# Kernel tuning notes

Measured on AMD Instinct MI355X. Metric: run time of the kernel, lower is better.

Reference implementation:

```python
import jax, jax.numpy as jnp
import numpy as np

D_MODEL = 1024
NUM_HEADS = 16
D_K = D_MODEL // NUM_HEADS


def setup_inputs() -> dict:
    key = jax.random.key(0)
    ks = jax.random.split(key, 9)
    s = 1.0 / np.sqrt(D_MODEL)
    x = jax.random.normal(ks[0], (2, 2048, D_MODEL), dtype=jnp.float32)
    Wq = jax.random.uniform(ks[1], (D_MODEL, D_MODEL), jnp.float32, -s, s)
    bq = jax.random.uniform(ks[2], (D_MODEL,), jnp.float32, -s, s)
    Wk = jax.random.uniform(ks[3], (D_MODEL, D_MODEL), jnp.float32, -s, s)
    bk = jax.random.uniform(ks[4], (D_MODEL,), jnp.float32, -s, s)
    Wv = jax.random.uniform(ks[5], (D_MODEL, D_MODEL), jnp.float32, -s, s)
    bv = jax.random.uniform(ks[6], (D_MODEL,), jnp.float32, -s, s)
    Wo = jax.random.uniform(ks[7], (D_MODEL, D_MODEL), jnp.float32, -s, s)
    bo = jax.random.uniform(ks[8], (D_MODEL,), jnp.float32, -s, s)
    return {"x": x, "Wq": Wq, "bq": bq, "Wk": Wk, "bk": bk,
            "Wv": Wv, "bv": bv, "Wo": Wo, "bo": bo}


def reference(x, Wq, bq, Wk, bk, Wv, bv, Wo, bo):
    B, S, _ = x.shape
    # torch Linear: y = x @ W.T + b
    def split_heads(t):
        return t.reshape(B, S, NUM_HEADS, D_K).transpose(0, 2, 1, 3)  # [B,H,S,Dk]
    Q = split_heads(x @ Wq.T + bq)
    K = split_heads(x @ Wk.T + bk)
    V = split_heads(x @ Wv.T + bv)
    scale = 1.0 / np.sqrt(D_K).astype(np.float32)
    scores = jnp.einsum('bhqd,bhkd->bhqk', Q, K) * scale  # [B,H,S,S]
    attn = jax.nn.softmax(scores, axis=-1)
    out = jnp.einsum('bhqk,bhkd->bhqd', attn, V)  # [B,H,S,Dk]
    out = out.transpose(0, 2, 1, 3).reshape(B, S, D_MODEL)
    return out @ Wo.T + bo
```

## Files before the change

### kernel.cpp

```cpp
#include <hip/hip_runtime.h>

constexpr int DMODEL = 1024;
constexpr int NHEAD  = 16;
constexpr int DKH    = 64;
constexpr int BATCH  = 2;
constexpr int SEQ    = 2048;
constexpr int MTOT   = BATCH * SEQ;
constexpr float SCL  = 0.18033688011112042f;

typedef __attribute__((ext_vector_type(8)))  short short8;
typedef __attribute__((ext_vector_type(4)))  float floatx4;
typedef __attribute__((ext_vector_type(16))) float floatx16;
typedef __attribute__((ext_vector_type(4)))  uint  uintx4;

__device__ __forceinline__ ushort f2bf(float f) {
    unsigned u = __builtin_bit_cast(unsigned, f);
    u = (u + 0x7fffu + ((u >> 16) & 1u)) >> 16;
    return (ushort)u;
}

__device__ __forceinline__ float exp2n(float x) {
#if __has_builtin(__builtin_amdgcn_exp2f)
    return __builtin_amdgcn_exp2f(x);
#else
    float r;
    asm("v_exp_f32 %0, %1" : "=v"(r) : "v"(x));
    return r;
#endif
}

__device__ __forceinline__ void gld16(const ushort* g, ushort* l) {
    __builtin_amdgcn_global_load_lds(
        (const __attribute__((address_space(1))) void*)g,
        (__attribute__((address_space(3))) void*)l, 16, 0, 0);
}

__global__ __launch_bounds__(256) void cvt_kernel(
    const float* __restrict__ x,  const float* __restrict__ wq,
    const float* __restrict__ wk, const float* __restrict__ wv,
    const float* __restrict__ wo,
    ushort* __restrict__ xb, ushort* __restrict__ wc, ushort* __restrict__ wob) {
    const int id = blockIdx.x * 256 + threadIdx.x;
    const float* src;
    ushort* dst;
    if (id < (1 << 20)) {
        src = x + (size_t)id * 4;
        dst = xb + (size_t)id * 4;
    } else {
        const int t = id - (1 << 20);
        const int seg = t >> 18;
        const size_t off = (size_t)(t & 0x3ffff) * 4;
        src = (seg == 0 ? wq : seg == 1 ? wk : seg == 2 ? wv : wo) + off;
        dst = (seg < 3) ? (wc + ((size_t)seg << 20) + off) : (wob + off);
    }
    const float4 v = *(const float4*)src;
    uint2 o;
    o.x = (uint)f2bf(v.x) | ((uint)f2bf(v.y) << 16);
    o.y = (uint)f2bf(v.z) | ((uint)f2bf(v.w) << 16);
    *(uint2*)dst = o;
}

template <int BMT, int MODE>
__global__ __launch_bounds__(256) void gemm_bf16(
    const ushort* __restrict__ A, const ushort* __restrict__ W,
    const float* __restrict__ bias0, const float* __restrict__ bias1,
    const float* __restrict__ bias2,
    ushort* __restrict__ Oq, ushort* __restrict__ Ok, ushort* __restrict__ Ov,
    float* __restrict__ Of) {
    constexpr int BM = 64 * BMT, BN = 128, BK = 64;
    constexpr int MI = 2 * BMT;
    constexpr int CA = BM / 8, CT = CA + BN / 8, NISS = CT / 4;
    constexpr int NKS = DMODEL / BK;
    __shared__ ushort Als[2][BM * BK];
    __shared__ ushort Bls[2][BN * BK];

    const int tid = threadIdx.x;
    const int w = tid >> 6, l = tid & 63;
    const int lr = l & 15, lg = l >> 4;
    const int wm = w >> 1, wn = w & 1;
    const int m0 = blockIdx.x * BM, n0 = blockIdx.y * BN;

    floatx4 acc[MI][4] = {};

    auto stage = [&](int ks, int buf) {
#pragma unroll
        for (int i = 0; i < NISS; i++) {
            const int c = w * NISS + i;
            const int cc = (c < CA) ? c : c - CA;
            const int row = (cc << 3) + (l >> 3);
            const int gcol = (((l & 7) ^ (row & 7)) << 3);
            if (c < CA)
                gld16(A + (size_t)(m0 + row) * DMODEL + ks * BK + gcol, &Als[buf][cc << 9]);
            else
                gld16(W + (size_t)(n0 + row) * DMODEL + ks * BK + gcol, &Bls[buf][cc << 9]);
        }
    };

    auto compute = [&](int buf) {
#pragma unroll
        for (int kk = 0; kk < 2; kk++) {
            short8 af[MI], bfv[4];
            const int u = kk * 4 + lg;
#pragma unroll
            for (int i = 0; i < MI; i++) {
                const int r = wm * (BM / 2) + i * 16 + lr;
                af[i] = *(const short8*)&Als[buf][r * 64 + ((u ^ (r & 7)) << 3)];
            }
#pragma unroll
            for (int j = 0; j < 4; j++) {
                const int r = wn * 64 + j * 16 + lr;
                bfv[j] = *(const short8*)&Bls[buf][r * 64 + ((u ^ (r & 7)) << 3)];
            }
            __builtin_amdgcn_s_setprio(1);
#pragma unroll
            for (int i = 0; i < MI; i++)
#pragma unroll
                for (int j = 0; j < 4; j++)
                    acc[i][j] = __builtin_amdgcn_mfma_f32_16x16x32_bf16(af[i], bfv[j], acc[i][j], 0, 0, 0);
            __builtin_amdgcn_s_setprio(0);
        }
    };

    stage(0, 0);
    __syncthreads();
#pragma unroll 1
    for (int ks = 0; ks < NKS - 1; ks++) {
        stage(ks + 1, (ks + 1) & 1);
        compute(ks & 1);
        __syncthreads();
    }
    compute((NKS - 1) & 1);

#pragma unroll
    for (int i = 0; i < MI; i++) {
        const int rbase = m0 + wm * (BM / 2) + i * 16 + lg * 4;
#pragma unroll
        for (int j = 0; j < 4; j++) {
            const int cg = n0 + wn * 64 + j * 16 + lr;
            if constexpr (MODE == 1) {
                const float bb = bias0[cg];
#pragma unroll
                for (int p = 0; p < 4; p++)
                    Of[(size_t)(rbase + p) * DMODEL + cg] = acc[i][j][p] + bb;
            } else {
                const int sel = cg >> 10, cw = cg & 1023;
                const int h = cw >> 6, d = cw & 63;
                const float bb = (sel == 0 ? bias0 : sel == 1 ? bias1 : bias2)[cw];
                const int b = rbase >> 11, s = rbase & (SEQ - 1);
                if (sel == 2) {
                    uint2 pk;
                    pk.x = (uint)f2bf(acc[i][j][0] + bb) | ((uint)f2bf(acc[i][j][1] + bb) << 16);
                    pk.y = (uint)f2bf(acc[i][j][2] + bb) | ((uint)f2bf(acc[i][j][3] + bb) << 16);
                    *(uint2*)&Ov[((size_t)(b * NHEAD + h) * DKH + d) * SEQ + s] = pk;
                } else if (sel == 0) {
                    uint2 pk;
                    pk.x = (uint)f2bf((acc[i][j][0] + bb) * SCL) |
                           ((uint)f2bf((acc[i][j][1] + bb) * SCL) << 16);
                    pk.y = (uint)f2bf((acc[i][j][2] + bb) * SCL) |
                           ((uint)f2bf((acc[i][j][3] + bb) * SCL) << 16);
                    *(uint2*)&Oq[((size_t)(b * NHEAD + h) * DKH + d) * SEQ + s] = pk;
                } else {
#pragma unroll
                    for (int p = 0; p < 4; p++)
                        Ok[((size_t)(b * NHEAD + h) * SEQ + s + p) * DKH + d] = f2bf(acc[i][j][p] + bb);
                }
            }
        }
    }
}

__global__ __launch_bounds__(512, 4) void attn_kernel(
    const ushort* __restrict__ Qt, const ushort* __restrict__ K,
    const ushort* __restrict__ Vt, ushort* __restrict__ O) {
    constexpr int KT = 64, NT = SEQ / KT, NTG = NT / 2;
    __shared__ ushort Kls[2][2][KT * 64];
    __shared__ ushort Vls[2][2][KT * 64];

    const int tid = threadIdx.x;
    const int w = tid >> 6, l = tid & 63;
    const int wl = w & 3, wg = w >> 2;
    const int q32 = l & 31, hl = l >> 5, l7 = l & 7;
    const int l0 = blockIdx.x;
    const int bh = (l0 & 7) + ((l0 >> 7) << 3);
    const int q0 = ((l0 >> 3) & 15) * 128;
    const int qb = q0 + wl * 32;
    const ushort* Qh = Qt + (size_t)bh * DKH * SEQ;
    const ushort* Kh = K  + (size_t)bh * SEQ * DKH;
    const ushort* Vh = Vt + (size_t)bh * DKH * SEQ;

    short8 qf[4];
#pragma unroll
    for (int c = 0; c < 4; c++)
#pragma unroll
        for (int j = 0; j < 8; j++)
            ((ushort*)&qf[c])[j] = Qh[(size_t)(16 * c + 8 * hl + j) * SEQ + qb + q32];

    short8 ones;
#pragma unroll
    for (int j = 0; j < 8; j++) ones[j] = (short)0x3F80;

    const int sr8 = l >> 3;
    const int scol = ((l & 7) ^ (sr8 & 7)) * 8;
    const ushort* Kg = Kh + (size_t)(wl * 16 + sr8) * DKH + scol;
    const ushort* Vg = Vh + (size_t)(wl * 16 + sr8) * SEQ + scol;

    floatx16 acc0 = {}, acc1 = {}, accl = {};

    auto stage = [&](int t, int buf) {
        ushort* kd = &Kls[wg][buf][0];
        ushort* vd = &Vls[wg][buf][0];
        gld16(Kg + (size_t)t * (KT * DKH),           kd + wl * 1024);
        gld16(Kg + (size_t)t * (KT * DKH) + 8 * DKH, kd + wl * 1024 + 512);
        gld16(Vg + (size_t)t * KT,                   vd + wl * 1024);
        gld16(Vg + (size_t)t * KT + 8 * SEQ,         vd + wl * 1024 + 512);
    };

    auto compute = [&](int buf) {
        const ushort* kb = &Kls[wg][buf][0];
        const ushort* vb = &Vls[wg][buf][0];
#pragma unroll
        for (int h = 0; h < 2; h++) {
            floatx16 sa = {};
            __builtin_amdgcn_s_setprio(1);
#pragma unroll
            for (int c = 0; c < 4; c++) {
                const int sl = (((2 * c + hl) ^ l7) << 3);
                const short8 kf = *(const short8*)&kb[(h * 32 + q32) * 64 + sl];
                sa = __builtin_amdgcn_mfma_f32_32x32x16_bf16(kf, qf[c], sa, 0, 0, 0);
            }
            __builtin_amdgcn_s_setprio(0);

#pragma unroll
            for (int i = 0; i < 16; i++) sa[i] = exp2n(sa[i]);

            uint wd[8];
#pragma unroll
            for (int m = 0; m < 8; m++)
                asm("v_cvt_pk_bf16_f32 %0, %1, %2"
                    : "=v"(wd[m]) : "v"(sa[2 * m]), "v"(sa[2 * m + 1]));
            asm volatile("v_permlane32_swap_b32 %0, %1" : "+v"(wd[0]), "+v"(wd[2]));
            asm volatile("v_permlane32_swap_b32 %0, %1" : "+v"(wd[1]), "+v"(wd[3]));
            asm volatile("v_permlane32_swap_b32 %0, %1" : "+v"(wd[4]), "+v"(wd[6]));
            asm volatile("v_permlane32_swap_b32 %0, %1" : "+v"(wd[5]), "+v"(wd[7]));
            uintx4 f0 = {wd[0], wd[1], wd[2], wd[3]};
            uintx4 f1 = {wd[4], wd[5], wd[6], wd[7]};
            const short8 pf0 = __builtin_bit_cast(short8, f0);
            const short8 pf1 = __builtin_bit_cast(short8, f1);

            __builtin_amdgcn_s_setprio(1);
#pragma unroll
            for (int c2 = 0; c2 < 2; c2++) {
                const int c = h * 2 + c2;
                const int sl = (((2 * c + hl) ^ l7) << 3);
                const short8 pfc = c2 ? pf1 : pf0;
                const short8 vf0 = *(const short8*)&vb[q32 * 64 + sl];
                const short8 vf1 = *(const short8*)&vb[(32 + q32) * 64 + sl];
                acc0 = __builtin_amdgcn_mfma_f32_32x32x16_bf16(vf0, pfc, acc0, 0, 0, 0);
                acc1 = __builtin_amdgcn_mfma_f32_32x32x16_bf16(vf1, pfc, acc1, 0, 0, 0);
                accl = __builtin_amdgcn_mfma_f32_32x32x16_bf16(ones, pfc, accl, 0, 0, 0);
            }
            __builtin_amdgcn_s_setprio(0);
        }
    };

    const int tb = wg * NTG;
    stage(tb, 0);
    __syncthreads();
#pragma unroll 1
    for (int it = 0; it < NTG / 2 - 1; it++) {
        stage(tb + 2 * it + 1, 1);
        compute(0);
        __syncthreads();
        stage(tb + 2 * it + 2, 0);
        compute(1);
        __syncthreads();
    }
    stage(tb + NTG - 1, 1);
    compute(0);
    __syncthreads();
    compute(1);

    __syncthreads();
    float* smA = (float*)&Kls[0][0][0];
    float* smB = (float*)&Vls[0][0][0];
    const int li = wl * 64 + l;
    if (wg == 1) {
        float* pa = smA + (size_t)li * 17;
        pa[0] = accl[0];
#pragma unroll
        for (int i = 0; i < 16; i++) pa[1 + i] = acc0[i];
        float* pb = smB + (size_t)li * 16;
#pragma unroll
        for (int i = 0; i < 16; i++) pb[i] = acc1[i];
    }
    __syncthreads();
    if (wg == 0) {
        const float* pa = smA + (size_t)li * 17;
        const float* pb = smB + (size_t)li * 16;
        const float inv = 1.0f / (accl[0] + pa[0]);
        const int b = bh >> 4, h = bh & (NHEAD - 1);
        ushort* Ob = O + (size_t)(b * SEQ + qb + q32) * DMODEL + h * DKH;
#pragma unroll
        for (int u = 0; u < 4; u++) {
            const float v0 = (acc0[4 * u]     + pa[1 + 4 * u])     * inv;
            const float v1 = (acc0[4 * u + 1] + pa[1 + 4 * u + 1]) * inv;
            const float v2 = (acc0[4 * u + 2] + pa[1 + 4 * u + 2]) * inv;
            const float v3 = (acc0[4 * u + 3] + pa[1 + 4 * u + 3]) * inv;
            uint2 pk;
            pk.x = (uint)f2bf(v0) | ((uint)f2bf(v1) << 16);
            pk.y = (uint)f2bf(v2) | ((uint)f2bf(v3) << 16);
            *(uint2*)&Ob[u * 8 + hl * 4] = pk;
        }
#pragma unroll
        for (int u = 0; u < 4; u++) {
            const float v0 = (acc1[4 * u]     + pb[4 * u])     * inv;
            const float v1 = (acc1[4 * u + 1] + pb[4 * u + 1]) * inv;
            const float v2 = (acc1[4 * u + 2] + pb[4 * u + 2]) * inv;
            const float v3 = (acc1[4 * u + 3] + pb[4 * u + 3]) * inv;
            uint2 pk;
            pk.x = (uint)f2bf(v0) | ((uint)f2bf(v1) << 16);
            pk.y = (uint)f2bf(v2) | ((uint)f2bf(v3) << 16);
            *(uint2*)&Ob[32 + u * 8 + hl * 4] = pk;
        }
    }
}

extern "C" void kernel_launch(void* const* d_in, const int* in_sizes, int n_in,
                              void* d_out, int out_size, void* d_ws, size_t ws_size,
                              hipStream_t stream) {
    const float* x  = (const float*)d_in[0];
    const float* Wq = (const float*)d_in[1];
    const float* bq = (const float*)d_in[2];
    const float* Wk = (const float*)d_in[3];
    const float* bk = (const float*)d_in[4];
    const float* Wv = (const float*)d_in[5];
    const float* bv = (const float*)d_in[6];
    const float* Wo = (const float*)d_in[7];
    const float* bo = (const float*)d_in[8];

    ushort* base = (ushort*)d_ws;
    ushort* xb  = base;
    ushort* wc  = xb  + (size_t)4 * 1024 * 1024;
    ushort* wob = wc  + (size_t)3 * 1024 * 1024;
    ushort* qws = wob + (size_t)1 * 1024 * 1024;
    ushort* kws = qws + (size_t)4 * 1024 * 1024;
    ushort* vws = kws + (size_t)4 * 1024 * 1024;
    ushort* aws = vws + (size_t)4 * 1024 * 1024;

    hipLaunchKernelGGL(cvt_kernel, dim3(8192), dim3(256), 0, stream,
                       x, Wq, Wk, Wv, Wo, xb, wc, wob);

    hipLaunchKernelGGL((gemm_bf16<2, 0>), dim3(MTOT / 128, 3072 / 128), dim3(256), 0, stream,
                       xb, wc, bq, bk, bv, qws, kws, vws, (float*)nullptr);

    hipLaunchKernelGGL(attn_kernel, dim3(512), dim3(512), 0, stream,
                       qws, kws, vws, aws);

    hipLaunchKernelGGL((gemm_bf16<1, 1>), dim3(MTOT / 64, DMODEL / 128), dim3(256), 0, stream,
                       aws, wob, bo, (const float*)nullptr, (const float*)nullptr,
                       (ushort*)nullptr, (ushort*)nullptr, (ushort*)nullptr, (float*)d_out);
}
```

Baseline: 99.45 us.

## Keep two global-to-LDS stages in flight with explicit vmcnt waits

Both the projection GEMM and the attention kernel now issue two stages of async global-to-LDS loads before the loop. Each iteration waits only until the older stage has landed (s_waitcnt vmcnt with a partial count) rather than draining every outstanding load at __syncthreads. The aim is deeper prefetch so memory latency overlaps with MFMA compute. It depends on NISS and the literal 4 exactly matching the number of loads each stage issues; if they do not, the wait count is wrong and the kernel reads stale LDS data.

Measured after the change: 100.5 us. No clear change (+1.1%).

```diff
diff --git a/kernel.cpp b/kernel.cpp
--- a/kernel.cpp
+++ b/kernel.cpp
@@ -28,6 +28,15 @@
     return r;
 #endif
 }
+
+#define VWAIT(N) do {                                            \
+    asm volatile("s_waitcnt vmcnt(%0)" :: "n"(N) : "memory");    \
+    __builtin_amdgcn_sched_barrier(0);                           \
+} while (0)
+#define SBAR() do {                                              \
+    __builtin_amdgcn_s_barrier();                                \
+    __builtin_amdgcn_sched_barrier(0);                           \
+} while (0)
 
 __device__ __forceinline__ void gld16(const ushort* g, ushort* l) {
     __builtin_amdgcn_global_load_lds(
@@ -122,13 +131,20 @@
     };
 
     stage(0, 0);
-    __syncthreads();
+    stage(1, 1);
 #pragma unroll 1
-    for (int ks = 0; ks < NKS - 1; ks++) {
-        stage(ks + 1, (ks + 1) & 1);
+    for (int ks = 0; ks < NKS - 2; ks++) {
+        VWAIT(NISS);
+        SBAR();
         compute(ks & 1);
-        __syncthreads();
-    }
+        SBAR();
+        stage(ks + 2, ks & 1);
+    }
+    VWAIT(NISS);
+    SBAR();
+    compute(NKS & 1);
+    VWAIT(0);
+    SBAR();
     compute((NKS - 1) & 1);
 
 #pragma unroll
@@ -265,20 +281,21 @@
 
     const int tb = wg * NTG;
     stage(tb, 0);
-    __syncthreads();
+    stage(tb + 1, 1);
 #pragma unroll 1
-    for (int it = 0; it < NTG / 2 - 1; it++) {
-        stage(tb + 2 * it + 1, 1);
-        compute(0);
-        __syncthreads();
-        stage(tb + 2 * it + 2, 0);
-        compute(1);
-        __syncthreads();
-    }
-    stage(tb + NTG - 1, 1);
-    compute(0);
-    __syncthreads();
-    compute(1);
+    for (int it = 0; it < NTG - 2; it++) {
+        VWAIT(4);
+        SBAR();
+        compute(it & 1);
+        SBAR();
+        stage(tb + it + 2, it & 1);
+    }
+    VWAIT(4);
+    SBAR();
+    compute(NTG & 1);
+    VWAIT(0);
+    SBAR();
+    compute((NTG - 1) & 1);
 
     __syncthreads();
     float* smA = (float*)&Kls[0][0][0];
```

## Compute softmax row sums with VALU adds and pad LDS tile layout

Applied to the files above, without the earlier changes.

Drops the extra MFMA against a ones vector that accumulated the softmax denominator. Each lane now sums its exponentials in fp32 and combines halves with a cross-lane shuffle. The K/V shared-memory tiles also get a padded chunk stride (528 elements) and a new XOR swizzle to avoid bank conflicts. This removes a third of the PV-stage matrix ops in exchange for VALU adds and a shuffle per half-tile. It also slightly changes summation precision, since the sum is now taken over fp32 values rather than bf16-rounded ones.

Result: slower. 101.5 us (+2.1%).

```diff
diff --git a/kernel.cpp b/kernel.cpp
--- a/kernel.cpp
+++ b/kernel.cpp
@@ -173,13 +173,15 @@
     const ushort* __restrict__ Qt, const ushort* __restrict__ K,
     const ushort* __restrict__ Vt, ushort* __restrict__ O) {
     constexpr int KT = 64, NT = SEQ / KT, NTG = NT / 2;
-    __shared__ ushort Kls[2][2][KT * 64];
-    __shared__ ushort Vls[2][2][KT * 64];
+    constexpr int CS = 528;
+    constexpr int TB = 8 * CS;
+    __shared__ ushort Kls[2][2][TB];
+    __shared__ ushort Vls[2][2][TB];
 
     const int tid = threadIdx.x;
     const int w = tid >> 6, l = tid & 63;
     const int wl = w & 3, wg = w >> 2;
-    const int q32 = l & 31, hl = l >> 5, l7 = l & 7;
+    const int q32 = l & 31, hl = l >> 5;
     const int l0 = blockIdx.x;
     const int bh = (l0 & 7) + ((l0 >> 7) << 3);
     const int q0 = ((l0 >> 3) & 15) * 128;
@@ -195,24 +197,27 @@
         for (int j = 0; j < 8; j++)
             ((ushort*)&qf[c])[j] = Qh[(size_t)(16 * c + 8 * hl + j) * SEQ + qb + q32];
 
-    short8 ones;
-#pragma unroll
-    for (int j = 0; j < 8; j++) ones[j] = (short)0x3F80;
-
-    const int sr8 = l >> 3;
-    const int scol = ((l & 7) ^ (sr8 & 7)) * 8;
-    const ushort* Kg = Kh + (size_t)(wl * 16 + sr8) * DKH + scol;
-    const ushort* Vg = Vh + (size_t)(wl * 16 + sr8) * SEQ + scol;
-
-    floatx16 acc0 = {}, acc1 = {}, accl = {};
+    const int rr8 = l >> 3;
+    const int sc0 = (((l & 7) ^ rr8 ^ ((2 * wl) & 3)) << 3);
+    const int sc1 = (((l & 7) ^ rr8 ^ ((2 * wl + 1) & 3)) << 3);
+    const ushort* Kg0 = Kh + (size_t)(wl * 16 + rr8) * DKH + sc0;
+    const ushort* Kg1 = Kh + (size_t)(wl * 16 + 8 + rr8) * DKH + sc1;
+    const ushort* Vg0 = Vh + (size_t)(wl * 16 + rr8) * SEQ + sc0;
+    const ushort* Vg1 = Vh + (size_t)(wl * 16 + 8 + rr8) * SEQ + sc1;
+
+    floatx16 acc0 = {}, acc1 = {};
+    float lsum = 0.f;
+
+    const int rbase = ((l >> 3) & 3) * CS + (l & 7) * 64;
+    const int bx = hl ^ (l & 7) ^ ((l >> 3) & 3);
 
     auto stage = [&](int t, int buf) {
         ushort* kd = &Kls[wg][buf][0];
         ushort* vd = &Vls[wg][buf][0];
-        gld16(Kg + (size_t)t * (KT * DKH),           kd + wl * 1024);
-        gld16(Kg + (size_t)t * (KT * DKH) + 8 * DKH, kd + wl * 1024 + 512);
-        gld16(Vg + (size_t)t * KT,                   vd + wl * 1024);
-        gld16(Vg + (size_t)t * KT + 8 * SEQ,         vd + wl * 1024 + 512);
+        gld16(Kg0 + (size_t)t * (KT * DKH), kd + (2 * wl) * CS);
+        gld16(Kg1 + (size_t)t * (KT * DKH), kd + (2 * wl + 1) * CS);
+        gld16(Vg0 + (size_t)t * KT,         vd + (2 * wl) * CS);
+        gld16(Vg1 + (size_t)t * KT,         vd + (2 * wl + 1) * CS);
     };
 
     auto compute = [&](int buf) {
@@ -224,14 +229,21 @@
             __builtin_amdgcn_s_setprio(1);
 #pragma unroll
             for (int c = 0; c < 4; c++) {
-                const int sl = (((2 * c + hl) ^ l7) << 3);
-                const short8 kf = *(const short8*)&kb[(h * 32 + q32) * 64 + sl];
+                const int sl = (((2 * c) ^ bx) << 3);
+                const short8 kf = *(const short8*)&kb[h * (4 * CS) + rbase + sl];
                 sa = __builtin_amdgcn_mfma_f32_32x32x16_bf16(kf, qf[c], sa, 0, 0, 0);
             }
             __builtin_amdgcn_s_setprio(0);
 
 #pragma unroll
             for (int i = 0; i < 16; i++) sa[i] = exp2n(sa[i]);
+
+            float ps = (((sa[0] + sa[1]) + (sa[2] + sa[3])) +
+                        ((sa[4] + sa[5]) + (sa[6] + sa[7]))) +
+                       (((sa[8] + sa[9]) + (sa[10] + sa[11])) +
+                        ((sa[12] + sa[13]) + (sa[14] + sa[15])));
+            ps += __shfl_xor(ps, 32);
+            lsum += ps;
 
             uint wd[8];
 #pragma unroll
@@ -251,13 +263,12 @@
 #pragma unroll
             for (int c2 = 0; c2 < 2; c2++) {
                 const int c = h * 2 + c2;
-                const int sl = (((2 * c + hl) ^ l7) << 3);
+                const int sl = (((2 * c) ^ bx) << 3);
                 const short8 pfc = c2 ? pf1 : pf0;
-                const short8 vf0 = *(const short8*)&vb[q32 * 64 + sl];
-                const short8 vf1 = *(const short8*)&vb[(32 + q32) * 64 + sl];
+                const short8 vf0 = *(const short8*)&vb[rbase + sl];
+                const short8 vf1 = *(const short8*)&vb[4 * CS + rbase + sl];
                 acc0 = __builtin_amdgcn_mfma_f32_32x32x16_bf16(vf0, pfc, acc0, 0, 0, 0);
                 acc1 = __builtin_amdgcn_mfma_f32_32x32x16_bf16(vf1, pfc, acc1, 0, 0, 0);
-                accl = __builtin_amdgcn_mfma_f32_32x32x16_bf16(ones, pfc, accl, 0, 0, 0);
             }
             __builtin_amdgcn_s_setprio(0);
         }
@@ -286,7 +297,7 @@
     const int li = wl * 64 + l;
     if (wg == 1) {
         float* pa = smA + (size_t)li * 17;
-        pa[0] = accl[0];
+        pa[0] = lsum;
 #pragma unroll
         for (int i = 0; i < 16; i++) pa[1 + i] = acc0[i];
         float* pb = smB + (size_t)li * 16;
@@ -297,7 +308,7 @@
     if (wg == 0) {
         const float* pa = smA + (size_t)li * 17;
         const float* pb = smB + (size_t)li * 16;
-        const float inv = 1.0f / (accl[0] + pa[0]);
+        const float inv = 1.0f / (lsum + pa[0]);
         const int b = bh >> 4, h = bh & (NHEAD - 1);
         ushort* Ob = O + (size_t)(b * SEQ + qb + q32) * DMODEL + h * DKH;
 #pragma unroll
```
